# Optimization experiments

Hardware: AMD Instinct MI355X
Metric: run time of the kernel (lower is better)

## Reference

```python
import jax, jax.numpy as jnp
import numpy as np

B, N, C, H = 4, 128, 512, 8
D = C // H
SCALE = D ** (-0.5) * 50.0


def setup_inputs() -> dict:
    key = jax.random.key(0)
    kx, kw = jax.random.split(key)
    x = jax.random.normal(kx, (B, N, N, C), dtype=jnp.float32)
    # torch Linear(n_embd, 5*n_embd, bias=False); stored here as [in, out] for x @ w
    w_qkv = jax.random.normal(kw, (C, 5 * C), dtype=jnp.float32) * (C ** -0.5)
    return {"x": x, "w_qkv": w_qkv}


def _heads(t):
    # [b, i, j, h*d] -> [b, h, i, j, d]
    b, i, j, _ = t.shape
    return t.reshape(b, i, j, H, D).transpose(0, 3, 1, 2, 4)


def reference(x, w_qkv):
    # global norm over the entire tensor (torch .std() is unbiased, ddof=1)
    x = (x - x.mean()) / x.std(ddof=1)
    qkv = x @ w_qkv                                   # [b, i, j, 5c]
    q, k1, k2, v1, v2 = map(_heads, jnp.split(qkv, 5, axis=-1))
    # pivotal attention: for query (i,j), pivot over k with row stream k1[i,k]
    # and column stream k2[k,j]
    scores = SCALE * (jnp.einsum('bhijd,bhikd->bhijk', q, k1)
                      + jnp.einsum('bhijd,bhkjd->bhijk', q, k2))
    attn = jax.nn.softmax(scores, axis=-1)            # [b, h, i, j, k]
    out = (jnp.einsum('bhijk,bhikd->bhijd', attn, v1)
           + jnp.einsum('bhijk,bhkjd->bhijd', attn, v2))
    # [b, h, i, j, d] -> [b, i, j, h*d]
    return out.transpose(0, 2, 3, 1, 4).reshape(B, N, N, C)
```

## Files before the change

kernel.cpp:

```cpp
#include <hip/hip_runtime.h>
#include <stdint.h>


typedef __attribute__((ext_vector_type(8))) short s8v;
typedef __attribute__((ext_vector_type(4))) float f4v;

#define MFMA(a, b, c) __builtin_amdgcn_mfma_f32_16x16x32_bf16((a), (b), (c), 0, 0, 0)

__device__ __forceinline__ float bf2f(unsigned short u) {
  union { unsigned int i; float f; } v; v.i = ((unsigned int)u) << 16; return v.f;
}
__device__ __forceinline__ unsigned short f2bf(float f) {
  union { float f; unsigned int i; } v; v.f = f;
  unsigned int i = v.i;
  return (unsigned short)((i + 0x7fffu + ((i >> 16) & 1u)) >> 16);
}

__device__ __forceinline__ void async_copy16(const void* g, void* l) {
  __builtin_amdgcn_global_load_lds(
      (const __attribute__((address_space(1))) unsigned int*)(uintptr_t)g,
      (__attribute__((address_space(3))) unsigned int*)(uintptr_t)l,
      16, 0, 0);
}

__global__ __launch_bounds__(256) void k_probe(const unsigned short* __restrict__ x,
                                               int* __restrict__ flag) {
  uint4 v = ((const uint4*)x)[threadIdx.x];
  unsigned int uu[4] = {v.x, v.y, v.z, v.w};
  int bad = 0;
#pragma unroll
  for (int u = 0; u < 4; ++u) {
    float a = bf2f((unsigned short)(uu[u] & 0xffffu));
    float b = bf2f((unsigned short)(uu[u] >> 16));
    if (!(fabsf(a) <= 1e4f)) bad = 1;
    if (!(fabsf(b) <= 1e4f)) bad = 1;
  }
  if (bad) atomicOr(flag, 1);
}

__global__ __launch_bounds__(256) void k_red(const void* __restrict__ xraw,
                                             const int* __restrict__ flag,
                                             double* __restrict__ dstats) {
  __shared__ float red[8];
  const int fm = flag[0];
  int t = threadIdx.x;
  size_t gid = (size_t)blockIdx.x * 256 + t;
  float s = 0.f, ss = 0.f;
  if (fm) {
    const float4* pf = (const float4*)xraw;
#pragma unroll 4
    for (int it = 0; it < 32; ++it) {
      size_t idx = gid + (size_t)it * 131072;
      float4 u1 = pf[2 * idx], u2 = pf[2 * idx + 1];
      float vals[8] = {u1.x, u1.y, u1.z, u1.w, u2.x, u2.y, u2.z, u2.w};
#pragma unroll
      for (int u = 0; u < 8; ++u) { s += vals[u]; ss += vals[u] * vals[u]; }
    }
  } else {
    const uint4* p = (const uint4*)xraw;
#pragma unroll 4
    for (int it = 0; it < 32; ++it) {
      uint4 v = p[gid + (size_t)it * 131072];
      unsigned int uu[4] = {v.x, v.y, v.z, v.w};
#pragma unroll
      for (int u = 0; u < 4; ++u) {
        float a = bf2f((unsigned short)(uu[u] & 0xffffu));
        float b = bf2f((unsigned short)(uu[u] >> 16));
        s += a + b;
        ss += a * a + b * b;
      }
    }
  }
#pragma unroll
  for (int d = 32; d >= 1; d >>= 1) {
    s += __shfl_down(s, d);
    ss += __shfl_down(ss, d);
  }
  int lane = t & 63, wave = t >> 6;
  if (lane == 0) { red[wave] = s; red[4 + wave] = ss; }
  __syncthreads();
  if (t == 0) {
    atomicAdd(&dstats[0], (double)(red[0] + red[1] + red[2] + red[3]));
    atomicAdd(&dstats[1], (double)(red[4] + red[5] + red[6] + red[7]));
  }
}

__global__ void k_stats(const double* __restrict__ dstats, float* __restrict__ fstats) {
  double M = 33554432.0;
  double mean = dstats[0] / M;
  double var = (dstats[1] - dstats[0] * dstats[0] / M) / (M - 1.0);
  double istd = 1.0 / sqrt(var);
  fstats[0] = (float)istd;
  fstats[1] = (float)(-mean * istd);
}

__global__ __launch_bounds__(256) void k_colsum(const void* __restrict__ wraw,
                                                const int* __restrict__ flag,
                                                float* __restrict__ colsum) {
  const int fm = flag[0];
  int c = blockIdx.x * 256 + threadIdx.x;
  if (c >= 2560) return;
  float s = 0.f;
  if (fm) {
    const float* w = (const float*)wraw;
    for (int r = 0; r < 512; ++r) s += w[(size_t)r * 2560 + c];
  } else {
    const unsigned short* w = (const unsigned short*)wraw;
    for (int r = 0; r < 512; ++r) s += bf2f(w[(size_t)r * 2560 + c]);
  }
  colsum[c] = s;
}

__global__ __launch_bounds__(256) void k_wt(const void* __restrict__ wraw,
                                            const int* __restrict__ flag,
                                            unsigned short* __restrict__ wThi,
                                            unsigned short* __restrict__ wTlo) {
  __shared__ float tile[64][65];
  const int fm = flag[0];
  int n0 = blockIdx.x * 64, r0 = blockIdx.y * 64;
#pragma unroll
  for (int rep = 0; rep < 16; ++rep) {
    int idx = rep * 256 + threadIdx.x;
    int r = idx >> 6, n = idx & 63;
    float v;
    if (fm) v = ((const float*)wraw)[(size_t)(r0 + r) * 2560 + n0 + n];
    else    v = bf2f(((const unsigned short*)wraw)[(size_t)(r0 + r) * 2560 + n0 + n]);
    tile[r][n] = v;
  }
  __syncthreads();
#pragma unroll
  for (int rep = 0; rep < 16; ++rep) {
    int idx = rep * 256 + threadIdx.x;
    int n = idx >> 6, r = idx & 63;
    float v = tile[r][n];
    unsigned short hi = f2bf(v);
    size_t o = (size_t)(n0 + n) * 512 + r0 + r;
    wThi[o] = hi;
    wTlo[o] = f2bf(v - bf2f(hi));
  }
}

__global__ __launch_bounds__(256) void k_convx(const void* __restrict__ xraw,
                                               const int* __restrict__ flag,
                                               unsigned short* __restrict__ xhi,
                                               unsigned short* __restrict__ xlo,
                                               int b) {
  const int fm = flag[0];
  size_t e0 = ((size_t)blockIdx.x * 256 + threadIdx.x) * 8;
  size_t g0 = (size_t)b * 8388608 + e0;
  float vals[8];
  if (fm) {
    const float4* pf = (const float4*)xraw;
    float4 u1 = pf[g0 / 4], u2 = pf[g0 / 4 + 1];
    vals[0] = u1.x; vals[1] = u1.y; vals[2] = u1.z; vals[3] = u1.w;
    vals[4] = u2.x; vals[5] = u2.y; vals[6] = u2.z; vals[7] = u2.w;
  } else {
    uint4 v = ((const uint4*)xraw)[g0 / 8];
    unsigned int uu[4] = {v.x, v.y, v.z, v.w};
#pragma unroll
    for (int u = 0; u < 4; ++u) {
      vals[2 * u] = bf2f((unsigned short)(uu[u] & 0xffffu));
      vals[2 * u + 1] = bf2f((unsigned short)(uu[u] >> 16));
    }
  }
  unsigned short h[8], l[8];
#pragma unroll
  for (int u = 0; u < 8; ++u) {
    h[u] = f2bf(vals[u]);
    l[u] = f2bf(vals[u] - bf2f(h[u]));
  }
  *(uint4*)(xhi + e0) = *(const uint4*)h;
  *(uint4*)(xlo + e0) = *(const uint4*)l;
}

__global__ __launch_bounds__(256) void k_gemm(
    const unsigned short* __restrict__ xhi, const unsigned short* __restrict__ xlo,
    const unsigned short* __restrict__ wThi, const unsigned short* __restrict__ wTlo,
    const float* __restrict__ colsum, const float* __restrict__ fstats,
    const int* __restrict__ flag,
    unsigned short* __restrict__ qhi, unsigned short* __restrict__ qlo,
    unsigned short* __restrict__ k1hi, unsigned short* __restrict__ k1lo,
    unsigned short* __restrict__ k2hi, unsigned short* __restrict__ k2lo,
    unsigned short* __restrict__ v1T, unsigned short* __restrict__ v2T,
    int h0, int hcShift) {
  __shared__ __align__(16) unsigned short Ash[128 * 64];
  __shared__ __align__(16) unsigned short Asl[128 * 64];
  __shared__ __align__(16) unsigned short Bsh[128 * 64];
  __shared__ __align__(16) unsigned short Bsl[128 * 64];
  const int fm = flag[0];
  const int t = threadIdx.x;
  const int m0 = blockIdx.x * 128;
  const int n0 = blockIdx.y * 128;
  const int hcMask = (1 << hcShift) - 1;

  const int lane = t & 63, wave = t >> 6;
  const int wm = (wave & 1) * 64, wn = (wave >> 1) * 64;
  const int l16 = lane & 15, q4 = lane >> 4;
  const int srow = t >> 3;
  const int scol = (t & 7) * 8;

  const float af = fstats[0], bfc = fstats[1];
  const unsigned short* xh = xhi + (size_t)m0 * 512;
  const unsigned short* xl = xlo + (size_t)m0 * 512;

  f4v acc[4][4];
#pragma unroll
  for (int a = 0; a < 4; ++a)
#pragma unroll
    for (int c = 0; c < 4; ++c) acc[a][c] = (f4v)0.f;

  for (int k0 = 0; k0 < 512; k0 += 64) {
#pragma unroll
    for (int r = 0; r < 4; ++r) {
      int row = r * 32 + srow;
      async_copy16(xh + (size_t)row * 512 + k0 + scol, (char*)Ash + (r * 256 + t) * 16);
    }
#pragma unroll
    for (int r = 0; r < 4; ++r) {
      int row = r * 32 + srow;
      int ncol = n0 + row;
      int g = ncol >> hcShift, rem = ncol & hcMask;
      int wcol = (g << 9) + ((h0 + (rem >> 6)) << 6) + (rem & 63);
      async_copy16(wThi + (size_t)wcol * 512 + k0 + scol, (char*)Bsh + (r * 256 + t) * 16);
    }
    if (fm) {
#pragma unroll
      for (int r = 0; r < 4; ++r) {
        int row = r * 32 + srow;
        async_copy16(xl + (size_t)row * 512 + k0 + scol, (char*)Asl + (r * 256 + t) * 16);
      }
#pragma unroll
      for (int r = 0; r < 4; ++r) {
        int row = r * 32 + srow;
        int ncol = n0 + row;
        int g = ncol >> hcShift, rem = ncol & hcMask;
        int wcol = (g << 9) + ((h0 + (rem >> 6)) << 6) + (rem & 63);
        async_copy16(wTlo + (size_t)wcol * 512 + k0 + scol, (char*)Bsl + (r * 256 + t) * 16);
      }
    }
    __syncthreads();
#pragma unroll
    for (int kc = 0; kc < 2; ++kc) {
      s8v ah[4], bh[4];
#pragma unroll
      for (int jt = 0; jt < 4; ++jt)
        ah[jt] = *(const s8v*)&Ash[(wm + jt * 16 + l16) * 64 + kc * 32 + q4 * 8];
#pragma unroll
      for (int nt = 0; nt < 4; ++nt)
        bh[nt] = *(const s8v*)&Bsh[(wn + nt * 16 + l16) * 64 + kc * 32 + q4 * 8];
      if (fm) {
        s8v al[4], bl[4];
#pragma unroll
        for (int jt = 0; jt < 4; ++jt)
          al[jt] = *(const s8v*)&Asl[(wm + jt * 16 + l16) * 64 + kc * 32 + q4 * 8];
#pragma unroll
        for (int nt = 0; nt < 4; ++nt)
          bl[nt] = *(const s8v*)&Bsl[(wn + nt * 16 + l16) * 64 + kc * 32 + q4 * 8];
#pragma unroll
        for (int jt = 0; jt < 4; ++jt)
#pragma unroll
          for (int nt = 0; nt < 4; ++nt) {
            acc[jt][nt] = MFMA(ah[jt], bh[nt], acc[jt][nt]);
            acc[jt][nt] = MFMA(ah[jt], bl[nt], acc[jt][nt]);
            acc[jt][nt] = MFMA(al[jt], bh[nt], acc[jt][nt]);
          }
      } else {
#pragma unroll
        for (int jt = 0; jt < 4; ++jt)
#pragma unroll
          for (int nt = 0; nt < 4; ++nt) acc[jt][nt] = MFMA(ah[jt], bh[nt], acc[jt][nt]);
      }
    }
    __syncthreads();
  }

#pragma unroll
  for (int jt = 0; jt < 4; ++jt) {
#pragma unroll
    for (int nt = 0; nt < 4; ++nt) {
      int gcol = n0 + wn + nt * 16 + l16;
      int g = gcol >> hcShift, rem = gcol & hcMask;
      int hl = rem >> 6, d = rem & 63;
      int wcol = (g << 9) + ((h0 + hl) << 6) + d;
      float cs = colsum[wcol] * bfc;
#pragma unroll
      for (int r = 0; r < 4; ++r) {
        int grow = m0 + wm + jt * 16 + q4 * 4 + r;
        int i = grow >> 7, j = grow & 127;
        float val = acc[jt][nt][r] * af + cs;
        unsigned short hi = f2bf(val);
        if (g == 0) {
          size_t idx = (((size_t)hl * 128 + i) * 128 + j) * 64 + d;
          qhi[idx] = hi; qlo[idx] = f2bf(val - bf2f(hi));
        } else if (g == 1) {
          size_t idx = (((size_t)hl * 128 + i) * 128 + j) * 64 + d;
          k1hi[idx] = hi; k1lo[idx] = f2bf(val - bf2f(hi));
        } else if (g == 2) {
          size_t idx = (((size_t)hl * 128 + j) * 128 + i) * 64 + d;
          k2hi[idx] = hi; k2lo[idx] = f2bf(val - bf2f(hi));
        } else if (g == 3) {
          size_t idx = (((size_t)hl * 128 + i) * 64 + d) * 128 + j;
          v1T[idx] = hi;
        } else {
          size_t idx = (((size_t)hl * 128 + j) * 64 + d) * 128 + i;
          v2T[idx] = hi;
        }
      }
    }
  }
}

__global__ __launch_bounds__(256) void k_s1(
    const unsigned short* __restrict__ qhi, const unsigned short* __restrict__ qlo,
    const unsigned short* __restrict__ k1hi, const unsigned short* __restrict__ k1lo,
    float* __restrict__ S) {
  const int i = blockIdx.x, hl = blockIdx.y;
  const int t = threadIdx.x, lane = t & 63, wave = t >> 6;
  const int l16 = lane & 15, q4 = lane >> 4;
  const size_t base = ((size_t)hl * 128 + i) * 128 * 64;

  f4v acc[2][8];
#pragma unroll
  for (int a = 0; a < 2; ++a)
#pragma unroll
    for (int c = 0; c < 8; ++c) acc[a][c] = (f4v)0.f;

#pragma unroll
  for (int kc = 0; kc < 2; ++kc) {
    s8v ah[2], al[2];
#pragma unroll
    for (int jt = 0; jt < 2; ++jt) {
      size_t off = base + (size_t)(wave * 32 + jt * 16 + l16) * 64 + kc * 32 + q4 * 8;
      ah[jt] = *(const s8v*)(qhi + off);
      al[jt] = *(const s8v*)(qlo + off);
    }
#pragma unroll
    for (int kt = 0; kt < 8; ++kt) {
      size_t off = base + (size_t)(kt * 16 + l16) * 64 + kc * 32 + q4 * 8;
      s8v bh = *(const s8v*)(k1hi + off);
      s8v bl = *(const s8v*)(k1lo + off);
#pragma unroll
      for (int jt = 0; jt < 2; ++jt) {
        acc[jt][kt] = MFMA(ah[jt], bh, acc[jt][kt]);
        acc[jt][kt] = MFMA(ah[jt], bl, acc[jt][kt]);
        acc[jt][kt] = MFMA(al[jt], bh, acc[jt][kt]);
      }
    }
  }
  float* Sb = S + ((size_t)hl * 128 + i) * 128 * 128;
#pragma unroll
  for (int jt = 0; jt < 2; ++jt)
#pragma unroll
    for (int kt = 0; kt < 8; ++kt)
#pragma unroll
      for (int r = 0; r < 4; ++r) {
        int j = wave * 32 + jt * 16 + q4 * 4 + r;
        Sb[(size_t)j * 128 + kt * 16 + l16] = acc[jt][kt][r];
      }
}

__global__ __launch_bounds__(256) void k_s2(
    const unsigned short* __restrict__ qhi, const unsigned short* __restrict__ qlo,
    const unsigned short* __restrict__ k2hi, const unsigned short* __restrict__ k2lo,
    const float* __restrict__ S, unsigned short* __restrict__ attn) {
  const int j = blockIdx.x, hl = blockIdx.y;
  const int t = threadIdx.x, lane = t & 63, wave = t >> 6;
  const int l16 = lane & 15, q4 = lane >> 4;
  const size_t bbase = ((size_t)hl * 128 + j) * 128 * 64;

  f4v acc[2][8];
#pragma unroll
  for (int a = 0; a < 2; ++a)
#pragma unroll
    for (int c = 0; c < 8; ++c) acc[a][c] = (f4v)0.f;

#pragma unroll
  for (int kc = 0; kc < 2; ++kc) {
    s8v ah[2], al[2];
#pragma unroll
    for (int it = 0; it < 2; ++it) {
      size_t off = (((size_t)hl * 128 + (wave * 32 + it * 16 + l16)) * 128 + j) * 64 +
                   kc * 32 + q4 * 8;
      ah[it] = *(const s8v*)(qhi + off);
      al[it] = *(const s8v*)(qlo + off);
    }
#pragma unroll
    for (int kt = 0; kt < 8; ++kt) {
      size_t off = bbase + (size_t)(kt * 16 + l16) * 64 + kc * 32 + q4 * 8;
      s8v bh = *(const s8v*)(k2hi + off);
      s8v bl = *(const s8v*)(k2lo + off);
#pragma unroll
      for (int it = 0; it < 2; ++it) {
        acc[it][kt] = MFMA(ah[it], bh, acc[it][kt]);
        acc[it][kt] = MFMA(ah[it], bl, acc[it][kt]);
        acc[it][kt] = MFMA(al[it], bh, acc[it][kt]);
      }
    }
  }

#pragma unroll
  for (int it = 0; it < 2; ++it) {
#pragma unroll
    for (int r = 0; r < 4; ++r) {
      int i = wave * 32 + it * 16 + q4 * 4 + r;
      const float* Srow = S + (((size_t)hl * 128 + i) * 128 + j) * 128;
      float tv[8];
      float m = -3.4e38f;
#pragma unroll
      for (int kt = 0; kt < 8; ++kt) {
        tv[kt] = 6.25f * (Srow[kt * 16 + l16] + acc[it][kt][r]);
        m = fmaxf(m, tv[kt]);
      }
#pragma unroll
      for (int d = 1; d <= 8; d <<= 1) m = fmaxf(m, __shfl_xor(m, d));
      float sum = 0.f;
#pragma unroll
      for (int kt = 0; kt < 8; ++kt) {
        tv[kt] = __expf(tv[kt] - m);
        sum += tv[kt];
      }
#pragma unroll
      for (int d = 1; d <= 8; d <<= 1) sum += __shfl_xor(sum, d);
      float rs = 1.f / sum;
      unsigned short* arow = attn + (((size_t)hl * 128 + i) * 128 + j) * 128;
#pragma unroll
      for (int kt = 0; kt < 8; ++kt) arow[kt * 16 + l16] = f2bf(tv[kt] * rs);
    }
  }
}

__global__ __launch_bounds__(256) void k_av1(
    const unsigned short* __restrict__ attn, const unsigned short* __restrict__ v1T,
    float* __restrict__ out1) {
  const int i = blockIdx.x, hl = blockIdx.y;
  const int t = threadIdx.x, lane = t & 63, wave = t >> 6;
  const int l16 = lane & 15, q4 = lane >> 4;
  const size_t abase = ((size_t)hl * 128 + i) * 128 * 128;
  const size_t vbase = ((size_t)hl * 128 + i) * 64 * 128;

  f4v acc[2][4];
#pragma unroll
  for (int a = 0; a < 2; ++a)
#pragma unroll
    for (int c = 0; c < 4; ++c) acc[a][c] = (f4v)0.f;

#pragma unroll
  for (int kc = 0; kc < 4; ++kc) {
    s8v a[2], bfr[4];
#pragma unroll
    for (int jt = 0; jt < 2; ++jt)
      a[jt] = *(const s8v*)(attn + abase + (size_t)(wave * 32 + jt * 16 + l16) * 128 +
                            kc * 32 + q4 * 8);
#pragma unroll
    for (int dt = 0; dt < 4; ++dt)
      bfr[dt] = *(const s8v*)(v1T + vbase + (size_t)(dt * 16 + l16) * 128 + kc * 32 + q4 * 8);
#pragma unroll
    for (int jt = 0; jt < 2; ++jt)
#pragma unroll
      for (int dt = 0; dt < 4; ++dt) acc[jt][dt] = MFMA(a[jt], bfr[dt], acc[jt][dt]);
  }
  float* ob = out1 + ((size_t)hl * 128 + i) * 128 * 64;
#pragma unroll
  for (int jt = 0; jt < 2; ++jt)
#pragma unroll
    for (int dt = 0; dt < 4; ++dt)
#pragma unroll
      for (int r = 0; r < 4; ++r) {
        int j = wave * 32 + jt * 16 + q4 * 4 + r;
        ob[(size_t)j * 64 + dt * 16 + l16] = acc[jt][dt][r];
      }
}

__global__ __launch_bounds__(256) void k_av2(
    const unsigned short* __restrict__ attn, const unsigned short* __restrict__ v2T,
    const float* __restrict__ out1, const int* __restrict__ flag,
    void* __restrict__ out, int b, int h0) {
  const int j = blockIdx.x, hl = blockIdx.y;
  const int t = threadIdx.x, lane = t & 63, wave = t >> 6;
  const int l16 = lane & 15, q4 = lane >> 4;
  const int fm = flag[0];
  const size_t vbase = ((size_t)hl * 128 + j) * 64 * 128;

  f4v acc[2][4];
#pragma unroll
  for (int a = 0; a < 2; ++a)
#pragma unroll
    for (int c = 0; c < 4; ++c) acc[a][c] = (f4v)0.f;

#pragma unroll
  for (int kc = 0; kc < 4; ++kc) {
    s8v a[2], bfr[4];
#pragma unroll
    for (int it = 0; it < 2; ++it)
      a[it] = *(const s8v*)(attn +
                            (((size_t)hl * 128 + (wave * 32 + it * 16 + l16)) * 128 + j) * 128 +
                            kc * 32 + q4 * 8);
#pragma unroll
    for (int dt = 0; dt < 4; ++dt)
      bfr[dt] = *(const s8v*)(v2T + vbase + (size_t)(dt * 16 + l16) * 128 + kc * 32 + q4 * 8);
#pragma unroll
    for (int it = 0; it < 2; ++it)
#pragma unroll
      for (int dt = 0; dt < 4; ++dt) acc[it][dt] = MFMA(a[it], bfr[dt], acc[it][dt]);
  }
#pragma unroll
  for (int it = 0; it < 2; ++it)
#pragma unroll
    for (int dt = 0; dt < 4; ++dt)
#pragma unroll
      for (int r = 0; r < 4; ++r) {
        int i = wave * 32 + it * 16 + q4 * 4 + r;
        int d = dt * 16 + l16;
        float o = acc[it][dt][r] + out1[(((size_t)hl * 128 + i) * 128 + j) * 64 + d];
        size_t oi = ((size_t)b * 16384 + i * 128 + j) * 512 + (h0 + hl) * 64 + d;
        if (fm) ((float*)out)[oi] = o;
        else    ((unsigned short*)out)[oi] = f2bf(o);
      }
}

extern "C" void kernel_launch(void* const* d_in, const int* in_sizes, int n_in,
                              void* d_out, int out_size, void* d_ws, size_t ws_size,
                              hipStream_t stream) {
  (void)in_sizes; (void)n_in; (void)out_size;
  const void* x = d_in[0];
  const void* w = d_in[1];

  const size_t xslice = (size_t)16384 * 512;
  const size_t wTsz = (size_t)2560 * 512;
  const size_t fixed = xslice * 4 + wTsz * 4 + 2560 * 4 + 64;

  int Hc = 2;
  if (32 * ((size_t)8 * 1048576) + fixed <= ws_size) Hc = 8;
  else if (32 * ((size_t)4 * 1048576) + fixed <= ws_size) Hc = 4;
  const int hcShift = (Hc == 8) ? 9 : ((Hc == 4) ? 8 : 7);
  const size_t TE = (size_t)Hc * 1048576;

  char* p = (char*)d_ws;
  unsigned short* qhi = (unsigned short*)p;  p += TE * 2;
  unsigned short* qlo = (unsigned short*)p;  p += TE * 2;
  unsigned short* k1hi = (unsigned short*)p; p += TE * 2;
  unsigned short* k1lo = (unsigned short*)p; p += TE * 2;
  unsigned short* k2hi = (unsigned short*)p; p += TE * 2;
  unsigned short* k2lo = (unsigned short*)p; p += TE * 2;
  unsigned short* v1T = (unsigned short*)p;  p += TE * 2;
  unsigned short* v2T = (unsigned short*)p;  p += TE * 2;
  float* S = (float*)p;                      p += TE * 8;
  unsigned short* attn = (unsigned short*)p; p += TE * 4;
  float* out1 = (float*)p;                   p += TE * 4;
  unsigned short* xhi = (unsigned short*)p;  p += xslice * 2;
  unsigned short* xlo = (unsigned short*)p;  p += xslice * 2;
  unsigned short* wThi = (unsigned short*)p; p += wTsz * 2;
  unsigned short* wTlo = (unsigned short*)p; p += wTsz * 2;
  float* colsum = (float*)p;                 p += 2560 * 4;
  double* dstats = (double*)p;               p += 16;
  int* flag = (int*)p;                       p += 8;
  float* fstats = (float*)p;                 p += 8;

  hipMemsetAsync(dstats, 0, 24, stream);
  k_probe<<<1, 256, 0, stream>>>((const unsigned short*)x, flag);
  k_red<<<512, 256, 0, stream>>>(x, flag, dstats);
  k_stats<<<1, 1, 0, stream>>>(dstats, fstats);
  k_colsum<<<10, 256, 0, stream>>>(w, flag, colsum);
  k_wt<<<dim3(40, 8), 256, 0, stream>>>(w, flag, wThi, wTlo);

  for (int b = 0; b < 4; ++b) {
    k_convx<<<4096, 256, 0, stream>>>(x, flag, xhi, xlo, b);
    for (int h0 = 0; h0 < 8; h0 += Hc) {
      k_gemm<<<dim3(128, (5 * Hc * 64) / 128), 256, 0, stream>>>(
          xhi, xlo, wThi, wTlo, colsum, fstats, flag,
          qhi, qlo, k1hi, k1lo, k2hi, k2lo, v1T, v2T, h0, hcShift);
      k_s1<<<dim3(128, Hc), 256, 0, stream>>>(qhi, qlo, k1hi, k1lo, S);
      k_s2<<<dim3(128, Hc), 256, 0, stream>>>(qhi, qlo, k2hi, k2lo, S, attn);
      k_av1<<<dim3(128, Hc), 256, 0, stream>>>(attn, v1T, out1);
      k_av2<<<dim3(128, Hc), 256, 0, stream>>>(attn, v2T, out1, flag, d_out, b, h0);
    }
  }
}
```

Measured before the change: 1.740 ms.

## Swizzle GEMM LDS tiles, hoist weight column indices, store out1 as bf16

```diff
diff --git a/kernel.cpp b/kernel.cpp
--- a/kernel.cpp
+++ b/kernel.cpp
@@ -197,12 +197,21 @@
   const int wm = (wave & 1) * 64, wn = (wave >> 1) * 64;
   const int l16 = lane & 15, q4 = lane >> 4;
   const int srow = t >> 3;
-  const int scol = (t & 7) * 8;
+  const int scol = (((t & 7) ^ ((t >> 3) & 7)) * 8);
+  const int rsw = l16 & 7;
 
   const float af = fstats[0], bfc = fstats[1];
   const unsigned short* xh = xhi + (size_t)m0 * 512;
   const unsigned short* xl = xlo + (size_t)m0 * 512;
 
+  int wcolr[4];
+#pragma unroll
+  for (int r = 0; r < 4; ++r) {
+    int ncol = n0 + r * 32 + srow;
+    int g = ncol >> hcShift, rem = ncol & hcMask;
+    wcolr[r] = (g << 9) + ((h0 + (rem >> 6)) << 6) + (rem & 63);
+  }
+
   f4v acc[4][4];
 #pragma unroll
   for (int a = 0; a < 4; ++a)
@@ -216,13 +225,8 @@
       async_copy16(xh + (size_t)row * 512 + k0 + scol, (char*)Ash + (r * 256 + t) * 16);
     }
 #pragma unroll
-    for (int r = 0; r < 4; ++r) {
-      int row = r * 32 + srow;
-      int ncol = n0 + row;
-      int g = ncol >> hcShift, rem = ncol & hcMask;
-      int wcol = (g << 9) + ((h0 + (rem >> 6)) << 6) + (rem & 63);
-      async_copy16(wThi + (size_t)wcol * 512 + k0 + scol, (char*)Bsh + (r * 256 + t) * 16);
-    }
+    for (int r = 0; r < 4; ++r)
+      async_copy16(wThi + (size_t)wcolr[r] * 512 + k0 + scol, (char*)Bsh + (r * 256 + t) * 16);
     if (fm) {
 #pragma unroll
       for (int r = 0; r < 4; ++r) {
@@ -230,32 +234,28 @@
         async_copy16(xl + (size_t)row * 512 + k0 + scol, (char*)Asl + (r * 256 + t) * 16);
       }
 #pragma unroll
-      for (int r = 0; r < 4; ++r) {
-        int row = r * 32 + srow;
-        int ncol = n0 + row;
-        int g = ncol >> hcShift, rem = ncol & hcMask;
-        int wcol = (g << 9) + ((h0 + (rem >> 6)) << 6) + (rem & 63);
-        async_copy16(wTlo + (size_t)wcol * 512 + k0 + scol, (char*)Bsl + (r * 256 + t) * 16);
-      }
+      for (int r = 0; r < 4; ++r)
+        async_copy16(wTlo + (size_t)wcolr[r] * 512 + k0 + scol, (char*)Bsl + (r * 256 + t) * 16);
     }
     __syncthreads();
 #pragma unroll
     for (int kc = 0; kc < 2; ++kc) {
+      const int swoff = ((kc * 4 + q4) ^ rsw) * 8;
       s8v ah[4], bh[4];
 #pragma unroll
       for (int jt = 0; jt < 4; ++jt)
-        ah[jt] = *(const s8v*)&Ash[(wm + jt * 16 + l16) * 64 + kc * 32 + q4 * 8];
+        ah[jt] = *(const s8v*)&Ash[(wm + jt * 16 + l16) * 64 + swoff];
 #pragma unroll
       for (int nt = 0; nt < 4; ++nt)
-        bh[nt] = *(const s8v*)&Bsh[(wn + nt * 16 + l16) * 64 + kc * 32 + q4 * 8];
+        bh[nt] = *(const s8v*)&Bsh[(wn + nt * 16 + l16) * 64 + swoff];
       if (fm) {
         s8v al[4], bl[4];
 #pragma unroll
         for (int jt = 0; jt < 4; ++jt)
-          al[jt] = *(const s8v*)&Asl[(wm + jt * 16 + l16) * 64 + kc * 32 + q4 * 8];
+          al[jt] = *(const s8v*)&Asl[(wm + jt * 16 + l16) * 64 + swoff];
 #pragma unroll
         for (int nt = 0; nt < 4; ++nt)
-          bl[nt] = *(const s8v*)&Bsl[(wn + nt * 16 + l16) * 64 + kc * 32 + q4 * 8];
+          bl[nt] = *(const s8v*)&Bsl[(wn + nt * 16 + l16) * 64 + swoff];
 #pragma unroll
         for (int jt = 0; jt < 4; ++jt)
 #pragma unroll
@@ -431,7 +431,7 @@
 
 __global__ __launch_bounds__(256) void k_av1(
     const unsigned short* __restrict__ attn, const unsigned short* __restrict__ v1T,
-    float* __restrict__ out1) {
+    unsigned short* __restrict__ out1) {
   const int i = blockIdx.x, hl = blockIdx.y;
   const int t = threadIdx.x, lane = t & 63, wave = t >> 6;
   const int l16 = lane & 15, q4 = lane >> 4;
@@ -459,7 +459,7 @@
 #pragma unroll
       for (int dt = 0; dt < 4; ++dt) acc[jt][dt] = MFMA(a[jt], bfr[dt], acc[jt][dt]);
   }
-  float* ob = out1 + ((size_t)hl * 128 + i) * 128 * 64;
+  unsigned short* ob = out1 + ((size_t)hl * 128 + i) * 128 * 64;
 #pragma unroll
   for (int jt = 0; jt < 2; ++jt)
 #pragma unroll
@@ -467,13 +467,13 @@
 #pragma unroll
       for (int r = 0; r < 4; ++r) {
         int j = wave * 32 + jt * 16 + q4 * 4 + r;
-        ob[(size_t)j * 64 + dt * 16 + l16] = acc[jt][dt][r];
+        ob[(size_t)j * 64 + dt * 16 + l16] = f2bf(acc[jt][dt][r]);
       }
 }
 
 __global__ __launch_bounds__(256) void k_av2(
     const unsigned short* __restrict__ attn, const unsigned short* __restrict__ v2T,
-    const float* __restrict__ out1, const int* __restrict__ flag,
+    const unsigned short* __restrict__ out1, const int* __restrict__ flag,
     void* __restrict__ out, int b, int h0) {
   const int j = blockIdx.x, hl = blockIdx.y;
   const int t = threadIdx.x, lane = t & 63, wave = t >> 6;
@@ -511,7 +511,7 @@
       for (int r = 0; r < 4; ++r) {
         int i = wave * 32 + it * 16 + q4 * 4 + r;
         int d = dt * 16 + l16;
-        float o = acc[it][dt][r] + out1[(((size_t)hl * 128 + i) * 128 + j) * 64 + d];
+        float o = acc[it][dt][r] + bf2f(out1[(((size_t)hl * 128 + i) * 128 + j) * 64 + d]);
         size_t oi = ((size_t)b * 16384 + i * 128 + j) * 512 + (h0 + hl) * 64 + d;
         if (fm) ((float*)out)[oi] = o;
         else    ((unsigned short*)out)[oi] = f2bf(o);
@@ -530,8 +530,8 @@
   const size_t fixed = xslice * 4 + wTsz * 4 + 2560 * 4 + 64;
 
   int Hc = 2;
-  if (32 * ((size_t)8 * 1048576) + fixed <= ws_size) Hc = 8;
-  else if (32 * ((size_t)4 * 1048576) + fixed <= ws_size) Hc = 4;
+  if (30 * ((size_t)8 * 1048576) + fixed <= ws_size) Hc = 8;
+  else if (30 * ((size_t)4 * 1048576) + fixed <= ws_size) Hc = 4;
   const int hcShift = (Hc == 8) ? 9 : ((Hc == 4) ? 8 : 7);
   const size_t TE = (size_t)Hc * 1048576;
 
@@ -546,7 +546,7 @@
   unsigned short* v2T = (unsigned short*)p;  p += TE * 2;
   float* S = (float*)p;                      p += TE * 8;
   unsigned short* attn = (unsigned short*)p; p += TE * 4;
-  float* out1 = (float*)p;                   p += TE * 4;
+  unsigned short* out1 = (unsigned short*)p; p += TE * 2;
   unsigned short* xhi = (unsigned short*)p;  p += xslice * 2;
   unsigned short* xlo = (unsigned short*)p;  p += xslice * 2;
   unsigned short* wThi = (unsigned short*)p; p += wTsz * 2;
```

New measurement: 1.649 ms. -5.2%, faster.
